# Performance work log

Measured on AMD Instinct MI355X. Metric: run time of the kernel, lower is better.

## Reference

```python
import jax, jax.numpy as jnp
import numpy as np

B, T, D, FF, H, K = 8, 1024, 512, 2048, 8, 15
HD = D // H  # key_dim = d_model // num_heads


def _ln(x, g, b):
    # keras LayerNormalization default epsilon = 1e-3
    m = jnp.mean(x, axis=-1, keepdims=True)
    v = jnp.var(x, axis=-1, keepdims=True)
    return (x - m) * jax.lax.rsqrt(v + 1e-3) * g + b


def setup_inputs() -> dict:
    key = jax.random.key(0)
    ks = iter(jax.random.split(key, 64))

    def rn(shape, s=0.02):
        return jax.random.normal(next(ks), shape, jnp.float32) * s

    p = {}
    p['x'] = jax.random.normal(next(ks), (B, T, D), jnp.float32)
    # ff_pre: LN -> Dense(FF, relu) -> Dense(D)
    p['g1'] = jnp.ones((D,), jnp.float32); p['b1'] = jnp.zeros((D,), jnp.float32)
    p['Wff1'] = rn((D, FF)); p['bff1'] = jnp.zeros((FF,), jnp.float32)
    p['Wff2'] = rn((FF, D)); p['bff2'] = jnp.zeros((D,), jnp.float32)
    # attention norm + MHA projections (keras EinsumDense shapes)
    p['ga'] = jnp.ones((D,), jnp.float32); p['ba'] = jnp.zeros((D,), jnp.float32)
    p['Wq'] = rn((D, H, HD)); p['bq'] = jnp.zeros((H, HD), jnp.float32)
    p['Wk'] = rn((D, H, HD)); p['bk'] = jnp.zeros((H, HD), jnp.float32)
    p['Wv'] = rn((D, H, HD)); p['bv'] = jnp.zeros((H, HD), jnp.float32)
    p['Wo'] = rn((H, HD, D)); p['bo'] = jnp.zeros((D,), jnp.float32)
    # conv branch: LN -> pointwise conv (2D, gelu) -> depthwise conv(k=15) -> BN -> swish -> pointwise conv (D)
    p['gc'] = jnp.ones((D,), jnp.float32); p['bc'] = jnp.zeros((D,), jnp.float32)
    p['Wcp'] = rn((D, 2 * D)); p['bcp'] = jnp.zeros((2 * D,), jnp.float32)
    p['dwk'] = rn((K, 1, 2 * D)); p['dwb'] = jnp.zeros((2 * D,), jnp.float32)
    p['bn_g'] = jnp.ones((2 * D,), jnp.float32); p['bn_b'] = jnp.zeros((2 * D,), jnp.float32)
    p['bn_m'] = jnp.zeros((2 * D,), jnp.float32)
    p['bn_v'] = jnp.ones((2 * D,), jnp.float32)
    p['Wco'] = rn((2 * D, D)); p['bco'] = jnp.zeros((D,), jnp.float32)
    # ff_post
    p['g2'] = jnp.ones((D,), jnp.float32); p['b2'] = jnp.zeros((D,), jnp.float32)
    p['Wf1'] = rn((D, FF)); p['bf1'] = jnp.zeros((FF,), jnp.float32)
    p['Wf2'] = rn((FF, D)); p['bf2'] = jnp.zeros((D,), jnp.float32)
    return p


def reference(x, g1, b1, Wff1, bff1, Wff2, bff2, ga, ba, Wq, bq, Wk, bk, Wv, bv, Wo, bo, gc, bc, Wcp, bcp, dwk, dwb, bn_g, bn_b, bn_m, bn_v, Wco, bco, g2, b2, Wf1, bf1, Wf2, bf2):
    # Macaron FFN (pre), half-step residual applied later
    x_ff = jnp.maximum(_ln(x, g1, b1) @ Wff1 + bff1, 0.0) @ Wff2 + bff2

    # causal multi-head self-attention (cache=None path)
    a = _ln(x, ga, ba)
    q = jnp.einsum('btd,dhk->bthk', a, Wq) + bq
    k = jnp.einsum('btd,dhk->bthk', a, Wk) + bk
    v = jnp.einsum('btd,dhk->bthk', a, Wv) + bv
    scores = jnp.einsum('bqhd,bkhd->bhqk', q, k) / jnp.sqrt(jnp.float32(HD))
    causal = jnp.tril(jnp.ones((T, T), bool))  # [T,T]
    scores = jnp.where(causal, scores, jnp.float32(-1e9))
    w = jax.nn.softmax(scores, axis=-1)
    ctx = jnp.einsum('bhqk,bkhd->bqhd', w, v)
    attn = jnp.einsum('bqhd,hdo->bqo', ctx, Wo) + bo

    x = x + 0.5 * x_ff + attn

    # convolution module: pointwise(gelu) -> causal left-pad -> depthwise -> BN(inference) -> swish -> pointwise
    c = jax.nn.gelu(_ln(x, gc, bc) @ Wcp + bcp, approximate=False)
    c = jnp.pad(c, ((0, 0), (K - 1, 0), (0, 0)))  # causal pad
    c = jax.lax.conv_general_dilated(
        c, dwk, window_strides=(1,), padding='VALID',
        dimension_numbers=('NWC', 'WIO', 'NWC'), feature_group_count=2 * D) + dwb
    c = (c - bn_m) * jax.lax.rsqrt(bn_v + 1e-3) * bn_g + bn_b
    c = c * jax.nn.sigmoid(c)  # swish
    c = c @ Wco + bco
    x = x + c

    # post FFN (full residual)
    x = x + (jnp.maximum(_ln(x, g2, b2) @ Wf1 + bf1, 0.0) @ Wf2 + bf2)
    return x
```

## Files before the change

kernel.cpp:

```cpp
#include <hip/hip_runtime.h>
#include <hip/hip_bf16.h>
#include <math.h>

#define BB 8
#define TT 1024
#define DD 512
#define FFD 2048
#define HH 8
#define HDD 64
#define KW 15
#define MR (BB*TT)
#define QKVN 1536

typedef __attribute__((ext_vector_type(8))) short short8;
typedef __attribute__((ext_vector_type(4))) short short4v;
typedef __attribute__((ext_vector_type(4))) float f32x4;
typedef __hip_bfloat16 bf16;

__device__ __forceinline__ float bf2f(unsigned u16) {
    return __uint_as_float(u16 << 16);
}

__device__ __forceinline__ void async_copy16(const void* g, void* l) {
    __builtin_amdgcn_global_load_lds(
        (const __attribute__((address_space(1))) void*)g,
        (__attribute__((address_space(3))) void*)l, 16, 0, 0);
}

__device__ __forceinline__ float gelu_exact(float v) {
    return 0.5f * v * (1.0f + erff(v * 0.70710678118654752f));
}

__global__ __launch_bounds__(256) void ln_kernel(const float* __restrict__ x,
                                                 const float* __restrict__ g,
                                                 const float* __restrict__ b,
                                                 bf16* __restrict__ out) {
    int wave = (blockIdx.x * blockDim.x + threadIdx.x) >> 6;
    int lane = threadIdx.x & 63;
    if (wave >= MR) return;
    const float* row = x + (size_t)wave * DD;
    float4 v0 = ((const float4*)row)[lane];
    float4 v1 = ((const float4*)row)[64 + lane];
    float s  = v0.x + v0.y + v0.z + v0.w + v1.x + v1.y + v1.z + v1.w;
    float ss = v0.x*v0.x + v0.y*v0.y + v0.z*v0.z + v0.w*v0.w
             + v1.x*v1.x + v1.y*v1.y + v1.z*v1.z + v1.w*v1.w;
    #pragma unroll
    for (int off = 32; off >= 1; off >>= 1) {
        s  += __shfl_xor(s,  off, 64);
        ss += __shfl_xor(ss, off, 64);
    }
    float mean = s * (1.0f / DD);
    float var  = ss * (1.0f / DD) - mean * mean;
    float r    = rsqrtf(var + 1e-3f);
    float4 g0 = ((const float4*)g)[lane];
    float4 g1 = ((const float4*)g)[64 + lane];
    float4 b0 = ((const float4*)b)[lane];
    float4 b1 = ((const float4*)b)[64 + lane];
    alignas(8) bf16 o0[4], o1[4];
    o0[0] = __float2bfloat16((v0.x - mean) * r * g0.x + b0.x);
    o0[1] = __float2bfloat16((v0.y - mean) * r * g0.y + b0.y);
    o0[2] = __float2bfloat16((v0.z - mean) * r * g0.z + b0.z);
    o0[3] = __float2bfloat16((v0.w - mean) * r * g0.w + b0.w);
    o1[0] = __float2bfloat16((v1.x - mean) * r * g1.x + b1.x);
    o1[1] = __float2bfloat16((v1.y - mean) * r * g1.y + b1.y);
    o1[2] = __float2bfloat16((v1.z - mean) * r * g1.z + b1.z);
    o1[3] = __float2bfloat16((v1.w - mean) * r * g1.w + b1.w);
    bf16* orow = out + (size_t)wave * DD;
    *(short4v*)(orow + lane * 4)       = *(const short4v*)o0;
    *(short4v*)(orow + 256 + lane * 4) = *(const short4v*)o1;
}

struct WtPack {
    const float* src[10];
    bf16*        dst[10];
    int          K[10];
    int          lgNT[10];
    float        scale[10];
    int          off[10];
};

__global__ __launch_bounds__(256) void wtrans_all_kernel(WtPack P) {
    __shared__ alignas(16) bf16 T[64][72];
    const int bid = blockIdx.x;
    int e = 0;
    #pragma unroll
    for (int i = 1; i < 10; ++i) e = (bid >= P.off[i]) ? i : e;
    const float* W  = P.src[e];
    bf16*        Wt = P.dst[e];
    const int    K  = P.K[e];
    const int    lg = P.lgNT[e];
    const float  scale = P.scale[e];
    const int local = bid - P.off[e];
    const int bx = local & ((1 << lg) - 1);
    const int by = local >> lg;
    const int k0 = by * 64;
    const int n0 = bx * 64;
    const int N  = (1 << lg) * 64;
    const int tid = threadIdx.x;
    #pragma unroll
    for (int it = 0; it < 4; ++it) {
        int lin = it * 256 + tid;
        int kl  = lin >> 4;
        int nq  = (lin & 15) * 4;
        float4 v = *(const float4*)(W + (size_t)(k0 + kl) * N + n0 + nq);
        T[nq + 0][kl] = __float2bfloat16(v.x * scale);
        T[nq + 1][kl] = __float2bfloat16(v.y * scale);
        T[nq + 2][kl] = __float2bfloat16(v.z * scale);
        T[nq + 3][kl] = __float2bfloat16(v.w * scale);
    }
    __syncthreads();
    #pragma unroll
    for (int it = 0; it < 4; ++it) {
        int lin = it * 256 + tid;
        int nl  = lin >> 4;
        int kq  = (lin & 15) * 4;
        *(short4v*)(Wt + (size_t)(n0 + nl) * K + k0 + kq) = *(const short4v*)&T[nl][kq];
    }
}

__global__ __launch_bounds__(256) void bconcat_kernel(const float* __restrict__ bq,
                                                      const float* __restrict__ bk,
                                                      const float* __restrict__ bv,
                                                      float* __restrict__ dst) {
    int i = blockIdx.x * 256 + threadIdx.x;
    float v = i < 512 ? bq[i] * 0.125f : (i < 1024 ? bk[i - 512] : bv[i - 1024]);
    dst[i] = v;
}

template<int BN, int OP, int RESMODE, int OUTMODE>
__global__ __launch_bounds__(256) void bgemm_kernel(
    const bf16* __restrict__ A,
    const bf16* __restrict__ Bt,
    const float* __restrict__ bias,
    const float* __restrict__ res1,
    const bf16* __restrict__ res2,
    float s2, float oscale,
    void* __restrict__ Cout,
    int N, int Kd, int nxb)
{
    constexpr int NT = BN / 32;
    __shared__ alignas(16) bf16 As[128][64];
    __shared__ alignas(16) bf16 Bs[BN][64];
    const int tid  = threadIdx.x;
    const int w    = tid >> 6;
    const int lane = tid & 63;
    const int quad = lane >> 4;
    const int l16  = lane & 15;
    const int wm   = w >> 1, wn = w & 1;

    const int flat = blockIdx.x;
    const int c8   = flat & 7;
    const int j    = flat >> 3;
    const int jy   = j / nxb;
    const int m0   = (c8 * 8 + jy) * 128;
    const int n0   = (j - jy * nxb) * BN;

    const int srow = lane >> 3;
    const int scol = ((lane & 7) ^ srow) * 8;

    const bf16* Ap = A  + (size_t)(m0 + w * 32 + srow) * Kd + scol;
    const bf16* Bp = Bt + (size_t)(n0 + w * (BN / 4) + srow) * Kd + scol;

    f32x4 acc[4][NT] = {};

    for (int k0 = 0; k0 < Kd; k0 += 64) {
        #pragma unroll
        for (int i = 0; i < 4; ++i)
            async_copy16(Ap + (size_t)(i * 8) * Kd + k0, &As[w * 32 + i * 8][0]);
        #pragma unroll
        for (int i = 0; i < BN / 32; ++i)
            async_copy16(Bp + (size_t)(i * 8) * Kd + k0, &Bs[w * (BN / 4) + i * 8][0]);
        __syncthreads();
        #pragma unroll
        for (int ks = 0; ks < 2; ++ks) {
            short8 af[4], bfr[NT];
            #pragma unroll
            for (int mt = 0; mt < 4; ++mt) {
                const int row = wm * 64 + mt * 16 + l16;
                const int c   = ((ks * 4 + quad) ^ (row & 7)) * 16;
                af[mt] = *(const short8*)((const char*)&As[row][0] + c);
            }
            #pragma unroll
            for (int nt = 0; nt < NT; ++nt) {
                const int col = wn * (BN / 2) + nt * 16 + l16;
                const int c   = ((ks * 4 + quad) ^ (col & 7)) * 16;
                bfr[nt] = *(const short8*)((const char*)&Bs[col][0] + c);
            }
            #pragma unroll
            for (int mt = 0; mt < 4; ++mt)
                #pragma unroll
                for (int nt = 0; nt < NT; ++nt)
                    acc[mt][nt] = __builtin_amdgcn_mfma_f32_16x16x32_bf16(
                        af[mt], bfr[nt], acc[mt][nt], 0, 0, 0);
        }
        __syncthreads();
    }

    const int crow0 = m0 + wm * 64 + quad * 4;
    const int ccol0 = n0 + wn * (BN / 2) + l16;
    #pragma unroll
    for (int nt = 0; nt < NT; ++nt) {
        const int col = ccol0 + nt * 16;
        const float bv = bias[col];
        #pragma unroll
        for (int mt = 0; mt < 4; ++mt) {
            #pragma unroll
            for (int r = 0; r < 4; ++r) {
                const int row = crow0 + mt * 16 + r;
                const size_t off = (size_t)row * N + col;
                float o = acc[mt][nt][r] + bv;
                if (OP == 1)      o = fmaxf(o, 0.f);
                else if (OP == 2) o = gelu_exact(o);
                if (RESMODE >= 1) o += res1[off];
                if (RESMODE == 2) o += s2 * __bfloat162float(res2[off]);
                if (OUTMODE == 0) ((float*)Cout)[off] = o;
                else              ((bf16*)Cout)[off]  = __float2bfloat16(o * oscale);
            }
        }
    }
}

__global__ __launch_bounds__(256) void vtrans_kernel(const bf16* __restrict__ qkv,
                                                     bf16* __restrict__ Vt) {
    __shared__ alignas(16) bf16 tile[64][264];
    int bh = blockIdx.x >> 2;
    int t0 = (blockIdx.x & 3) * 256;
    int b = bh >> 3, h = bh & 7;
    int tid = threadIdx.x;
    #pragma unroll
    for (int it = 0; it < 16; ++it) {
        int lin = it * 256 + tid;
        int tl  = lin >> 4;
        int seg = lin & 15;
        short4v val = *(const short4v*)(qkv + ((size_t)(b * TT) + t0 + tl) * QKVN
                                        + 1024 + h * 64 + seg * 4);
        tile[seg * 4 + 0][tl] = ((const bf16*)&val)[0];
        tile[seg * 4 + 1][tl] = ((const bf16*)&val)[1];
        tile[seg * 4 + 2][tl] = ((const bf16*)&val)[2];
        tile[seg * 4 + 3][tl] = ((const bf16*)&val)[3];
    }
    __syncthreads();
    #pragma unroll
    for (int it = 0; it < 16; ++it) {
        int lin = it * 256 + tid;
        int d   = lin >> 6;
        int tq  = (lin & 63) * 4;
        *(short4v*)(Vt + ((size_t)bh * 64 + d) * TT + t0 + tq) =
            *(const short4v*)&tile[d][tq];
    }
}

__global__ __launch_bounds__(256) void fattn_kernel(
    const bf16* __restrict__ QKV,
    const bf16* __restrict__ Vt,
    bf16* __restrict__ ctx)
{
    __shared__ alignas(16) bf16 Ks[2][64][64];
    __shared__ alignas(16) bf16 Vs[2][64][64];
    const int tid  = threadIdx.x;
    const int w    = tid >> 6;
    const int lane = tid & 63;
    const int quad = lane >> 4;
    const int l16  = lane & 15;
    const int bh   = blockIdx.x & 63;
    const int bi   = 15 - (blockIdx.x >> 6);
    const int b = bh >> 3, h = bh & 7;

    const bf16* Qg = QKV + (size_t)(b * TT) * QKVN + h * 64;
    const bf16* Kg = QKV + (size_t)(b * TT) * QKVN + 512 + h * 64;
    const bf16* Vg = Vt  + (size_t)bh * 64 * TT;

    const int qw = bi * 64 + w * 16;
    short8 qf0 = *(const short8*)(Qg + (size_t)(qw + l16) * QKVN + quad * 8);
    short8 qf1 = *(const short8*)(Qg + (size_t)(qw + l16) * QKVN + 32 + quad * 8);

    const int sgrow  = lane >> 3;
    const int sgchnk = lane & 7;

    f32x4 cacc[4] = {};
    float l_lane = 0.f;
    const int prow_base = ((l16 >> 2) << 3) + (l16 & 3);

    #pragma unroll
    for (int i = 0; i < 2; ++i) {
        const int rowbase = w * 8 + i * 32;
        const int row = rowbase + sgrow;
        const int fR = (row & 3) | (((row >> 3) & 1) << 2);
        const int sc = sgchnk ^ fR;
        async_copy16(Kg + (size_t)row * QKVN + sc * 8, &Ks[0][rowbase][0]);
        async_copy16(Vg + (size_t)row * TT + sc * 8,   &Vs[0][rowbase][0]);
    }

    int buf = 0;
    for (int s = 0; s <= bi; ++s) {
        __syncthreads();
        if (s < bi) {
            const int kn = (s + 1) * 64;
            #pragma unroll
            for (int i = 0; i < 2; ++i) {
                const int rowbase = w * 8 + i * 32;
                const int row = rowbase + sgrow;
                const int fR = (row & 3) | (((row >> 3) & 1) << 2);
                const int sc = sgchnk ^ fR;
                async_copy16(Kg + (size_t)(kn + row) * QKVN + sc * 8, &Ks[buf ^ 1][rowbase][0]);
                async_copy16(Vg + (size_t)row * TT + kn + sc * 8,     &Vs[buf ^ 1][rowbase][0]);
            }
        }
        const int k0 = s * 64;

        f32x4 sT[4];
        #pragma unroll
        for (int s4 = 0; s4 < 4; ++s4) {
            const int prow = prow_base + (s4 >> 1) * 32 + (s4 & 1) * 4;
            const int fR = (prow & 3) | (((prow >> 3) & 1) << 2);
            short8 ka = *(const short8*)&Ks[buf][prow][(quad ^ fR) * 8];
            short8 kb = *(const short8*)&Ks[buf][prow][((4 + quad) ^ fR) * 8];
            f32x4 z = {0.f, 0.f, 0.f, 0.f};
            z = __builtin_amdgcn_mfma_f32_16x16x32_bf16(ka, qf0, z, 0, 0, 0);
            sT[s4] = __builtin_amdgcn_mfma_f32_16x16x32_bf16(kb, qf1, z, 0, 0, 0);
        }

        alignas(16) bf16 pb[16];
        if (s == bi) {
            const int qglob = qw + l16;
            #pragma unroll
            for (int s4 = 0; s4 < 4; ++s4)
                #pragma unroll
                for (int r = 0; r < 4; ++r) {
                    const int key = k0 + (s4 >> 1) * 32 + quad * 8 + (s4 & 1) * 4 + r;
                    const float p = (key <= qglob) ? __expf(sT[s4][r]) : 0.f;
                    l_lane += p;
                    pb[s4 * 4 + r] = __float2bfloat16(p);
                }
        } else {
            #pragma unroll
            for (int s4 = 0; s4 < 4; ++s4)
                #pragma unroll
                for (int r = 0; r < 4; ++r) {
                    const float p = __expf(sT[s4][r]);
                    l_lane += p;
                    pb[s4 * 4 + r] = __float2bfloat16(p);
                }
        }
        const short8 pf0 = *(const short8*)&pb[0];
        const short8 pf1 = *(const short8*)&pb[8];

        #pragma unroll
        for (int g = 0; g < 4; ++g) {
            const int vrow = g * 16 + l16;
            const int fR = (vrow & 3) | (((vrow >> 3) & 1) << 2);
            short8 va = *(const short8*)&Vs[buf][vrow][(quad ^ fR) * 8];
            short8 vb = *(const short8*)&Vs[buf][vrow][((4 + quad) ^ fR) * 8];
            cacc[g] = __builtin_amdgcn_mfma_f32_16x16x32_bf16(va, pf0, cacc[g], 0, 0, 0);
            cacc[g] = __builtin_amdgcn_mfma_f32_16x16x32_bf16(vb, pf1, cacc[g], 0, 0, 0);
        }
        buf ^= 1;
    }

    l_lane += __shfl_xor(l_lane, 16, 64);
    l_lane += __shfl_xor(l_lane, 32, 64);
    const float inv = 1.0f / l_lane;

    bf16* Cb = ctx + (size_t)(b * TT + qw + l16) * DD + h * 64;
    #pragma unroll
    for (int g = 0; g < 4; ++g) {
        alignas(8) bf16 o[4];
        #pragma unroll
        for (int r = 0; r < 4; ++r) o[r] = __float2bfloat16(cacc[g][r] * inv);
        *(short4v*)(Cb + g * 16 + quad * 4) = *(const short4v*)o;
    }
}

__global__ __launch_bounds__(256) void dwconv_kernel(const bf16* __restrict__ c1,
                                                     const float* __restrict__ dwk,
                                                     const float* __restrict__ dwb,
                                                     const float* __restrict__ bn_g,
                                                     const float* __restrict__ bn_b,
                                                     const float* __restrict__ bn_m,
                                                     const float* __restrict__ bn_v,
                                                     bf16* __restrict__ out) {
    const int C2 = 2 * DD;
    const int lin = blockIdx.x * 256 + threadIdx.x;
    const int chp = lin & 511;
    const int ch  = chp << 1;
    const int tch = lin >> 9;
    const int row0 = tch << 3;
    const int t0   = row0 & (TT - 1);

    float w0[KW], w1[KW];
    #pragma unroll
    for (int i = 0; i < KW; ++i) {
        w0[i] = dwk[i * C2 + ch];
        w1[i] = dwk[i * C2 + ch + 1];
    }
    const float a0 = rsqrtf(bn_v[ch] + 1e-3f) * bn_g[ch];
    const float a1 = rsqrtf(bn_v[ch + 1] + 1e-3f) * bn_g[ch + 1];
    const float c0 = (dwb[ch] - bn_m[ch]) * a0 + bn_b[ch];
    const float c1v = (dwb[ch + 1] - bn_m[ch + 1]) * a1 + bn_b[ch + 1];

    float x0[22], x1[22];
    if (t0 >= KW - 1) {
        #pragma unroll
        for (int i = 0; i < 22; ++i) {
            unsigned u = *(const unsigned*)(c1 + (size_t)(row0 - (KW - 1) + i) * C2 + ch);
            x0[i] = bf2f(u & 0xffff);
            x1[i] = bf2f(u >> 16);
        }
    } else {
        #pragma unroll
        for (int i = 0; i < 22; ++i) {
            unsigned u = 0;
            if (t0 - (KW - 1) + i >= 0)
                u = *(const unsigned*)(c1 + (size_t)(row0 - (KW - 1) + i) * C2 + ch);
            x0[i] = bf2f(u & 0xffff);
            x1[i] = bf2f(u >> 16);
        }
    }

    #pragma unroll
    for (int j = 0; j < 8; ++j) {
        float s0 = 0.f, s1 = 0.f;
        #pragma unroll
        for (int i = 0; i < KW; ++i) {
            s0 += x0[j + i] * w0[i];
            s1 += x1[j + i] * w1[i];
        }
        s0 = s0 * a0 + c0;
        s1 = s1 * a1 + c1v;
        s0 = s0 / (1.f + __expf(-s0));
        s1 = s1 / (1.f + __expf(-s1));
        alignas(4) bf16 ob[2] = {__float2bfloat16(s0), __float2bfloat16(s1)};
        *(unsigned*)(out + (size_t)(row0 + j) * C2 + ch) = *(const unsigned*)ob;
    }
}

extern "C" void kernel_launch(void* const* d_in, const int* in_sizes, int n_in,
                              void* d_out, int out_size, void* d_ws, size_t ws_size,
                              hipStream_t stream) {
    const float* x    = (const float*)d_in[0];
    const float* g1   = (const float*)d_in[1];
    const float* b1   = (const float*)d_in[2];
    const float* Wff1 = (const float*)d_in[3];
    const float* bff1 = (const float*)d_in[4];
    const float* Wff2 = (const float*)d_in[5];
    const float* bff2 = (const float*)d_in[6];
    const float* ga   = (const float*)d_in[7];
    const float* ba   = (const float*)d_in[8];
    const float* Wq   = (const float*)d_in[9];
    const float* bq   = (const float*)d_in[10];
    const float* Wk   = (const float*)d_in[11];
    const float* bk   = (const float*)d_in[12];
    const float* Wv   = (const float*)d_in[13];
    const float* bv   = (const float*)d_in[14];
    const float* Wo   = (const float*)d_in[15];
    const float* bo   = (const float*)d_in[16];
    const float* gc   = (const float*)d_in[17];
    const float* bc   = (const float*)d_in[18];
    const float* Wcp  = (const float*)d_in[19];
    const float* bcp  = (const float*)d_in[20];
    const float* dwk  = (const float*)d_in[21];
    const float* dwb  = (const float*)d_in[22];
    const float* bn_g = (const float*)d_in[23];
    const float* bn_b = (const float*)d_in[24];
    const float* bn_m = (const float*)d_in[25];
    const float* bn_v = (const float*)d_in[26];
    const float* Wco  = (const float*)d_in[27];
    const float* bco  = (const float*)d_in[28];
    const float* g2   = (const float*)d_in[29];
    const float* b2   = (const float*)d_in[30];
    const float* Wf1  = (const float*)d_in[31];
    const float* bf1  = (const float*)d_in[32];
    const float* Wf2  = (const float*)d_in[33];
    const float* bf2  = (const float*)d_in[34];

    float* out = (float*)d_out;

    char* p = (char*)d_ws;
    bf16* lnb   = (bf16*)p;  p += (size_t)MR * DD * 2;
    bf16* qkvb  = (bf16*)p;  p += (size_t)MR * QKVN * 2;
    bf16* Vtb   = (bf16*)p;  p += (size_t)MR * DD * 2;
    bf16* ctxb  = (bf16*)p;  p += (size_t)MR * DD * 2;
    bf16* xffb  = (bf16*)p;  p += (size_t)MR * DD * 2;
    bf16* bigb  = (bf16*)p;  p += (size_t)MR * FFD * 2;
    bf16* c2b   = (bf16*)p;  p += (size_t)MR * 1024 * 2;
    bf16* Wff1t = (bf16*)p;  p += (size_t)FFD * DD * 2;
    bf16* Wff2t = (bf16*)p;  p += (size_t)DD * FFD * 2;
    bf16* Wqkvt = (bf16*)p;  p += (size_t)QKVN * DD * 2;
    bf16* Wot   = (bf16*)p;  p += (size_t)DD * DD * 2;
    bf16* Wcpt  = (bf16*)p;  p += (size_t)1024 * DD * 2;
    bf16* Wcot  = (bf16*)p;  p += (size_t)DD * 1024 * 2;
    bf16* Wf1t  = (bf16*)p;  p += (size_t)FFD * DD * 2;
    bf16* Wf2t  = (bf16*)p;  p += (size_t)DD * FFD * 2;
    float* bqkv = (float*)p; p += QKVN * 4;

    dim3 blk(256);
    dim3 ln_grid(MR / 4);

    WtPack P;
    auto set = [&](int i, const float* s, bf16* d, int K, int N, float sc, int off) {
        P.src[i] = s; P.dst[i] = d; P.K[i] = K; P.scale[i] = sc; P.off[i] = off;
        int nt = N / 64, lg = 0; while ((1 << lg) < nt) ++lg; P.lgNT[i] = lg;
    };
    set(0, Wff1, Wff1t, DD,  FFD, 1.f,    0);
    set(1, Wff2, Wff2t, FFD, DD,  1.f,    256);
    set(2, Wq,   Wqkvt,                DD, DD, 0.125f, 512);
    set(3, Wk,   Wqkvt + (size_t)512 * DD,  DD, DD, 1.f, 576);
    set(4, Wv,   Wqkvt + (size_t)1024 * DD, DD, DD, 1.f, 640);
    set(5, Wo,   Wot,   DD,  DD,  1.f,    704);
    set(6, Wcp,  Wcpt,  DD,  1024, 1.f,   768);
    set(7, Wco,  Wcot,  1024, DD, 1.f,    896);
    set(8, Wf1,  Wf1t,  DD,  FFD, 1.f,    1024);
    set(9, Wf2,  Wf2t,  FFD, DD,  1.f,    1280);
    wtrans_all_kernel<<<dim3(1536), blk, 0, stream>>>(P);
    bconcat_kernel<<<dim3(QKVN / 256), blk, 0, stream>>>(bq, bk, bv, bqkv);

    ln_kernel<<<ln_grid, blk, 0, stream>>>(x, g1, b1, lnb);
    bgemm_kernel<128, 1, 0, 1><<<dim3(16 * 64), blk, 0, stream>>>(
        lnb, Wff1t, bff1, nullptr, nullptr, 0.f, 1.f, bigb, FFD, DD, 16);
    bgemm_kernel<64, 0, 0, 1><<<dim3(8 * 64), blk, 0, stream>>>(
        bigb, Wff2t, bff2, nullptr, nullptr, 0.f, 1.f, xffb, DD, FFD, 8);
    ln_kernel<<<ln_grid, blk, 0, stream>>>(x, ga, ba, lnb);
    bgemm_kernel<128, 0, 0, 1><<<dim3(12 * 64), blk, 0, stream>>>(
        lnb, Wqkvt, bqkv, nullptr, nullptr, 0.f, 1.f, qkvb, QKVN, DD, 12);
    vtrans_kernel<<<dim3(64 * 4), blk, 0, stream>>>(qkvb, Vtb);
    fattn_kernel<<<dim3(64 * 16), blk, 0, stream>>>(qkvb, Vtb, ctxb);
    bgemm_kernel<64, 0, 2, 0><<<dim3(8 * 64), blk, 0, stream>>>(
        ctxb, Wot, bo, x, xffb, 0.5f, 1.f, out, DD, DD, 8);
    ln_kernel<<<ln_grid, blk, 0, stream>>>(out, gc, bc, lnb);
    bgemm_kernel<128, 2, 0, 1><<<dim3(8 * 64), blk, 0, stream>>>(
        lnb, Wcpt, bcp, nullptr, nullptr, 0.f, 1.f, bigb, 1024, DD, 8);
    dwconv_kernel<<<dim3(MR * 512 / 8 / 256), blk, 0, stream>>>(
        bigb, dwk, dwb, bn_g, bn_b, bn_m, bn_v, c2b);
    bgemm_kernel<64, 0, 1, 0><<<dim3(8 * 64), blk, 0, stream>>>(
        c2b, Wcot, bco, out, nullptr, 0.f, 1.f, out, DD, 1024, 8);
    ln_kernel<<<ln_grid, blk, 0, stream>>>(out, g2, b2, lnb);
    bgemm_kernel<128, 1, 0, 1><<<dim3(16 * 64), blk, 0, stream>>>(
        lnb, Wf1t, bf1, nullptr, nullptr, 0.f, 1.f, bigb, FFD, DD, 16);
    bgemm_kernel<64, 0, 1, 0><<<dim3(8 * 64), blk, 0, stream>>>(
        bigb, Wf2t, bf2, out, nullptr, 0.f, 1.f, out, DD, FFD, 8);
}
```

Measured before the change: 399.1 us.

## Fuse LN pair, bias concat, V transpose; process two query tiles per attention block

```diff
diff --git a/kernel.cpp b/kernel.cpp
--- a/kernel.cpp
+++ b/kernel.cpp
@@ -29,6 +29,72 @@
 
 __device__ __forceinline__ float gelu_exact(float v) {
     return 0.5f * v * (1.0f + erff(v * 0.70710678118654752f));
+}
+
+__global__ __launch_bounds__(256) void ln_dual_kernel(const float* __restrict__ x,
+                                                      const float* __restrict__ g1,
+                                                      const float* __restrict__ b1,
+                                                      const float* __restrict__ ga,
+                                                      const float* __restrict__ ba,
+                                                      bf16* __restrict__ o1,
+                                                      bf16* __restrict__ o2) {
+    int wave = (blockIdx.x * blockDim.x + threadIdx.x) >> 6;
+    int lane = threadIdx.x & 63;
+    if (wave >= MR) return;
+    const float* row = x + (size_t)wave * DD;
+    float4 v0 = ((const float4*)row)[lane];
+    float4 v1 = ((const float4*)row)[64 + lane];
+    float s  = v0.x + v0.y + v0.z + v0.w + v1.x + v1.y + v1.z + v1.w;
+    float ss = v0.x*v0.x + v0.y*v0.y + v0.z*v0.z + v0.w*v0.w
+             + v1.x*v1.x + v1.y*v1.y + v1.z*v1.z + v1.w*v1.w;
+    #pragma unroll
+    for (int off = 32; off >= 1; off >>= 1) {
+        s  += __shfl_xor(s,  off, 64);
+        ss += __shfl_xor(ss, off, 64);
+    }
+    float mean = s * (1.0f / DD);
+    float var  = ss * (1.0f / DD) - mean * mean;
+    float r    = rsqrtf(var + 1e-3f);
+    float n0x = (v0.x - mean) * r, n0y = (v0.y - mean) * r,
+          n0z = (v0.z - mean) * r, n0w = (v0.w - mean) * r;
+    float n1x = (v1.x - mean) * r, n1y = (v1.y - mean) * r,
+          n1z = (v1.z - mean) * r, n1w = (v1.w - mean) * r;
+    {
+        float4 g0 = ((const float4*)g1)[lane];
+        float4 gg1 = ((const float4*)g1)[64 + lane];
+        float4 b0 = ((const float4*)b1)[lane];
+        float4 bb1 = ((const float4*)b1)[64 + lane];
+        alignas(8) bf16 oo0[4], oo1[4];
+        oo0[0] = __float2bfloat16(n0x * g0.x + b0.x);
+        oo0[1] = __float2bfloat16(n0y * g0.y + b0.y);
+        oo0[2] = __float2bfloat16(n0z * g0.z + b0.z);
+        oo0[3] = __float2bfloat16(n0w * g0.w + b0.w);
+        oo1[0] = __float2bfloat16(n1x * gg1.x + bb1.x);
+        oo1[1] = __float2bfloat16(n1y * gg1.y + bb1.y);
+        oo1[2] = __float2bfloat16(n1z * gg1.z + bb1.z);
+        oo1[3] = __float2bfloat16(n1w * gg1.w + bb1.w);
+        bf16* orow = o1 + (size_t)wave * DD;
+        *(short4v*)(orow + lane * 4)       = *(const short4v*)oo0;
+        *(short4v*)(orow + 256 + lane * 4) = *(const short4v*)oo1;
+    }
+    {
+        float4 g0 = ((const float4*)ga)[lane];
+        float4 gg1 = ((const float4*)ga)[64 + lane];
+        float4 b0 = ((const float4*)ba)[lane];
+        float4 bb1 = ((const float4*)ba)[64 + lane];
+        alignas(8) bf16 oo0[4], oo1[4];
+        oo0[0] = __float2bfloat16(n0x * g0.x + b0.x);
+        oo0[1] = __float2bfloat16(n0y * g0.y + b0.y);
+        oo0[2] = __float2bfloat16(n0z * g0.z + b0.z);
+        oo0[3] = __float2bfloat16(n0w * g0.w + b0.w);
+        oo1[0] = __float2bfloat16(n1x * gg1.x + bb1.x);
+        oo1[1] = __float2bfloat16(n1y * gg1.y + bb1.y);
+        oo1[2] = __float2bfloat16(n1z * gg1.z + bb1.z);
+        oo1[3] = __float2bfloat16(n1w * gg1.w + bb1.w);
+        bf16* orow = o2 + (size_t)wave * DD;
+        *(short4v*)(orow + lane * 4)       = *(const short4v*)oo0;
+        *(short4v*)(orow + 256 + lane * 4) = *(const short4v*)oo1;
+    }
 }
 
 __global__ __launch_bounds__(256) void ln_kernel(const float* __restrict__ x,
@@ -77,11 +143,23 @@
     int          lgNT[10];
     float        scale[10];
     int          off[10];
+    const float* bq; const float* bk; const float* bv;
+    float*       bdst;
 };
 
 __global__ __launch_bounds__(256) void wtrans_all_kernel(WtPack P) {
     __shared__ alignas(16) bf16 T[64][72];
     const int bid = blockIdx.x;
+    if (bid >= 1536) {
+        #pragma unroll
+        for (int it = 0; it < 6; ++it) {
+            int i = it * 256 + threadIdx.x;
+            float v = i < 512 ? P.bq[i] * 0.125f
+                              : (i < 1024 ? P.bk[i - 512] : P.bv[i - 1024]);
+            P.bdst[i] = v;
+        }
+        return;
+    }
     int e = 0;
     #pragma unroll
     for (int i = 1; i < 10; ++i) e = (bid >= P.off[i]) ? i : e;
@@ -118,15 +196,6 @@
     }
 }
 
-__global__ __launch_bounds__(256) void bconcat_kernel(const float* __restrict__ bq,
-                                                      const float* __restrict__ bk,
-                                                      const float* __restrict__ bv,
-                                                      float* __restrict__ dst) {
-    int i = blockIdx.x * 256 + threadIdx.x;
-    float v = i < 512 ? bq[i] * 0.125f : (i < 1024 ? bk[i - 512] : bv[i - 1024]);
-    dst[i] = v;
-}
-
 template<int BN, int OP, int RESMODE, int OUTMODE>
 __global__ __launch_bounds__(256) void bgemm_kernel(
     const bf16* __restrict__ A,
@@ -134,6 +203,7 @@
     const float* __restrict__ bias,
     const float* __restrict__ res1,
     const bf16* __restrict__ res2,
+    bf16* __restrict__ aux,
     float s2, float oscale,
     void* __restrict__ Cout,
     int N, int Kd, int nxb)
@@ -204,49 +274,38 @@
         const float bv = bias[col];
         #pragma unroll
         for (int mt = 0; mt < 4; ++mt) {
-            #pragma unroll
-            for (int r = 0; r < 4; ++r) {
-                const int row = crow0 + mt * 16 + r;
-                const size_t off = (size_t)row * N + col;
-                float o = acc[mt][nt][r] + bv;
-                if (OP == 1)      o = fmaxf(o, 0.f);
-                else if (OP == 2) o = gelu_exact(o);
-                if (RESMODE >= 1) o += res1[off];
-                if (RESMODE == 2) o += s2 * __bfloat162float(res2[off]);
-                if (OUTMODE == 0) ((float*)Cout)[off] = o;
-                else              ((bf16*)Cout)[off]  = __float2bfloat16(o * oscale);
+            if (OUTMODE == 2) {
+                alignas(8) bf16 o4[4];
+                #pragma unroll
+                for (int r = 0; r < 4; ++r)
+                    o4[r] = __float2bfloat16((acc[mt][nt][r] + bv) * oscale);
+                if (col < 1024) {
+                    #pragma unroll
+                    for (int r = 0; r < 4; ++r)
+                        ((bf16*)Cout)[(size_t)(crow0 + mt * 16 + r) * N + col] = o4[r];
+                } else {
+                    const int dg   = col - 1024;
+                    const int rowt = crow0 + mt * 16;
+                    const int b2   = rowt >> 10, t0 = rowt & 1023;
+                    const int bh2  = b2 * 8 + (dg >> 6), d = dg & 63;
+                    *(short4v*)(aux + ((size_t)bh2 * 64 + d) * TT + t0) =
+                        *(const short4v*)o4;
+                }
+            } else {
+                #pragma unroll
+                for (int r = 0; r < 4; ++r) {
+                    const int row = crow0 + mt * 16 + r;
+                    const size_t off = (size_t)row * N + col;
+                    float o = acc[mt][nt][r] + bv;
+                    if (OP == 1)      o = fmaxf(o, 0.f);
+                    else if (OP == 2) o = gelu_exact(o);
+                    if (RESMODE >= 1) o += res1[off];
+                    if (RESMODE == 2) o += s2 * __bfloat162float(res2[off]);
+                    if (OUTMODE == 0) ((float*)Cout)[off] = o;
+                    else              ((bf16*)Cout)[off]  = __float2bfloat16(o * oscale);
+                }
             }
         }
-    }
-}
-
-__global__ __launch_bounds__(256) void vtrans_kernel(const bf16* __restrict__ qkv,
-                                                     bf16* __restrict__ Vt) {
-    __shared__ alignas(16) bf16 tile[64][264];
-    int bh = blockIdx.x >> 2;
-    int t0 = (blockIdx.x & 3) * 256;
-    int b = bh >> 3, h = bh & 7;
-    int tid = threadIdx.x;
-    #pragma unroll
-    for (int it = 0; it < 16; ++it) {
-        int lin = it * 256 + tid;
-        int tl  = lin >> 4;
-        int seg = lin & 15;
-        short4v val = *(const short4v*)(qkv + ((size_t)(b * TT) + t0 + tl) * QKVN
-                                        + 1024 + h * 64 + seg * 4);
-        tile[seg * 4 + 0][tl] = ((const bf16*)&val)[0];
-        tile[seg * 4 + 1][tl] = ((const bf16*)&val)[1];
-        tile[seg * 4 + 2][tl] = ((const bf16*)&val)[2];
-        tile[seg * 4 + 3][tl] = ((const bf16*)&val)[3];
-    }
-    __syncthreads();
-    #pragma unroll
-    for (int it = 0; it < 16; ++it) {
-        int lin = it * 256 + tid;
-        int d   = lin >> 6;
-        int tq  = (lin & 63) * 4;
-        *(short4v*)(Vt + ((size_t)bh * 64 + d) * TT + t0 + tq) =
-            *(const short4v*)&tile[d][tq];
     }
 }
 
@@ -263,23 +322,27 @@
     const int quad = lane >> 4;
     const int l16  = lane & 15;
     const int bh   = blockIdx.x & 63;
-    const int bi   = 15 - (blockIdx.x >> 6);
+    const int bi   = 7 - (blockIdx.x >> 6);
     const int b = bh >> 3, h = bh & 7;
 
     const bf16* Qg = QKV + (size_t)(b * TT) * QKVN + h * 64;
     const bf16* Kg = QKV + (size_t)(b * TT) * QKVN + 512 + h * 64;
     const bf16* Vg = Vt  + (size_t)bh * 64 * TT;
 
-    const int qw = bi * 64 + w * 16;
-    short8 qf0 = *(const short8*)(Qg + (size_t)(qw + l16) * QKVN + quad * 8);
-    short8 qf1 = *(const short8*)(Qg + (size_t)(qw + l16) * QKVN + 32 + quad * 8);
+    const int qL = bi * 128 + w * 16;
+    const int qH = qL + 64;
+    short8 qfL0 = *(const short8*)(Qg + (size_t)(qL + l16) * QKVN + quad * 8);
+    short8 qfL1 = *(const short8*)(Qg + (size_t)(qL + l16) * QKVN + 32 + quad * 8);
+    short8 qfH0 = *(const short8*)(Qg + (size_t)(qH + l16) * QKVN + quad * 8);
+    short8 qfH1 = *(const short8*)(Qg + (size_t)(qH + l16) * QKVN + 32 + quad * 8);
 
     const int sgrow  = lane >> 3;
     const int sgchnk = lane & 7;
 
-    f32x4 cacc[4] = {};
-    float l_lane = 0.f;
+    f32x4 caccL[4] = {}, caccH[4] = {};
+    float lL = 0.f, lH = 0.f;
     const int prow_base = ((l16 >> 2) << 3) + (l16 & 3);
+    const int smax = 2 * bi + 1;
 
     #pragma unroll
     for (int i = 0; i < 2; ++i) {
@@ -292,9 +355,9 @@
     }
 
     int buf = 0;
-    for (int s = 0; s <= bi; ++s) {
+    for (int s = 0; s <= smax; ++s) {
         __syncthreads();
-        if (s < bi) {
+        if (s < smax) {
             const int kn = (s + 1) * 64;
             #pragma unroll
             for (int i = 0; i < 2; ++i) {
@@ -307,43 +370,74 @@
             }
         }
         const int k0 = s * 64;
-
-        f32x4 sT[4];
+        const bool doL = (s < smax);
+
+        f32x4 sTL[4], sTH[4];
         #pragma unroll
         for (int s4 = 0; s4 < 4; ++s4) {
             const int prow = prow_base + (s4 >> 1) * 32 + (s4 & 1) * 4;
             const int fR = (prow & 3) | (((prow >> 3) & 1) << 2);
             short8 ka = *(const short8*)&Ks[buf][prow][(quad ^ fR) * 8];
             short8 kb = *(const short8*)&Ks[buf][prow][((4 + quad) ^ fR) * 8];
-            f32x4 z = {0.f, 0.f, 0.f, 0.f};
-            z = __builtin_amdgcn_mfma_f32_16x16x32_bf16(ka, qf0, z, 0, 0, 0);
-            sT[s4] = __builtin_amdgcn_mfma_f32_16x16x32_bf16(kb, qf1, z, 0, 0, 0);
-        }
-
-        alignas(16) bf16 pb[16];
-        if (s == bi) {
-            const int qglob = qw + l16;
+            f32x4 zH = {0.f, 0.f, 0.f, 0.f};
+            zH = __builtin_amdgcn_mfma_f32_16x16x32_bf16(ka, qfH0, zH, 0, 0, 0);
+            sTH[s4] = __builtin_amdgcn_mfma_f32_16x16x32_bf16(kb, qfH1, zH, 0, 0, 0);
+            if (doL) {
+                f32x4 zL = {0.f, 0.f, 0.f, 0.f};
+                zL = __builtin_amdgcn_mfma_f32_16x16x32_bf16(ka, qfL0, zL, 0, 0, 0);
+                sTL[s4] = __builtin_amdgcn_mfma_f32_16x16x32_bf16(kb, qfL1, zL, 0, 0, 0);
+            }
+        }
+
+        alignas(16) bf16 pbH[16], pbL[16];
+        if (s == smax) {
+            const int qg = qH + l16;
             #pragma unroll
             for (int s4 = 0; s4 < 4; ++s4)
                 #pragma unroll
                 for (int r = 0; r < 4; ++r) {
                     const int key = k0 + (s4 >> 1) * 32 + quad * 8 + (s4 & 1) * 4 + r;
-                    const float p = (key <= qglob) ? __expf(sT[s4][r]) : 0.f;
-                    l_lane += p;
-                    pb[s4 * 4 + r] = __float2bfloat16(p);
+                    const float p = (key <= qg) ? __expf(sTH[s4][r]) : 0.f;
+                    lH += p;
+                    pbH[s4 * 4 + r] = __float2bfloat16(p);
                 }
         } else {
             #pragma unroll
             for (int s4 = 0; s4 < 4; ++s4)
                 #pragma unroll
                 for (int r = 0; r < 4; ++r) {
-                    const float p = __expf(sT[s4][r]);
-                    l_lane += p;
-                    pb[s4 * 4 + r] = __float2bfloat16(p);
+                    const float p = __expf(sTH[s4][r]);
+                    lH += p;
+                    pbH[s4 * 4 + r] = __float2bfloat16(p);
                 }
         }
-        const short8 pf0 = *(const short8*)&pb[0];
-        const short8 pf1 = *(const short8*)&pb[8];
+        if (doL) {
+            if (s == smax - 1) {
+                const int qg = qL + l16;
+                #pragma unroll
+                for (int s4 = 0; s4 < 4; ++s4)
+                    #pragma unroll
+                    for (int r = 0; r < 4; ++r) {
+                        const int key = k0 + (s4 >> 1) * 32 + quad * 8 + (s4 & 1) * 4 + r;
+                        const float p = (key <= qg) ? __expf(sTL[s4][r]) : 0.f;
+                        lL += p;
+                        pbL[s4 * 4 + r] = __float2bfloat16(p);
+                    }
+            } else {
+                #pragma unroll
+                for (int s4 = 0; s4 < 4; ++s4)
+                    #pragma unroll
+                    for (int r = 0; r < 4; ++r) {
+                        const float p = __expf(sTL[s4][r]);
+                        lL += p;
+                        pbL[s4 * 4 + r] = __float2bfloat16(p);
+                    }
+            }
+        }
+        const short8 pfH0 = *(const short8*)&pbH[0];
+        const short8 pfH1 = *(const short8*)&pbH[8];
+        const short8 pfL0 = *(const short8*)&pbL[0];
+        const short8 pfL1 = *(const short8*)&pbL[8];
 
         #pragma unroll
         for (int g = 0; g < 4; ++g) {
@@ -351,23 +445,35 @@
             const int fR = (vrow & 3) | (((vrow >> 3) & 1) << 2);
             short8 va = *(const short8*)&Vs[buf][vrow][(quad ^ fR) * 8];
             short8 vb = *(const short8*)&Vs[buf][vrow][((4 + quad) ^ fR) * 8];
-            cacc[g] = __builtin_amdgcn_mfma_f32_16x16x32_bf16(va, pf0, cacc[g], 0, 0, 0);
-            cacc[g] = __builtin_amdgcn_mfma_f32_16x16x32_bf16(vb, pf1, cacc[g], 0, 0, 0);
+            caccH[g] = __builtin_amdgcn_mfma_f32_16x16x32_bf16(va, pfH0, caccH[g], 0, 0, 0);
+            caccH[g] = __builtin_amdgcn_mfma_f32_16x16x32_bf16(vb, pfH1, caccH[g], 0, 0, 0);
+            if (doL) {
+                caccL[g] = __builtin_amdgcn_mfma_f32_16x16x32_bf16(va, pfL0, caccL[g], 0, 0, 0);
+                caccL[g] = __builtin_amdgcn_mfma_f32_16x16x32_bf16(vb, pfL1, caccL[g], 0, 0, 0);
+            }
         }
         buf ^= 1;
     }
 
-    l_lane += __shfl_xor(l_lane, 16, 64);
-    l_lane += __shfl_xor(l_lane, 32, 64);
-    const float inv = 1.0f / l_lane;
-
-    bf16* Cb = ctx + (size_t)(b * TT + qw + l16) * DD + h * 64;
+    lL += __shfl_xor(lL, 16, 64);
+    lL += __shfl_xor(lL, 32, 64);
+    lH += __shfl_xor(lH, 16, 64);
+    lH += __shfl_xor(lH, 32, 64);
+    const float invL = 1.0f / lL;
+    const float invH = 1.0f / lH;
+
+    bf16* CbL = ctx + (size_t)(b * TT + qL + l16) * DD + h * 64;
+    bf16* CbH = ctx + (size_t)(b * TT + qH + l16) * DD + h * 64;
     #pragma unroll
     for (int g = 0; g < 4; ++g) {
-        alignas(8) bf16 o[4];
-        #pragma unroll
-        for (int r = 0; r < 4; ++r) o[r] = __float2bfloat16(cacc[g][r] * inv);
-        *(short4v*)(Cb + g * 16 + quad * 4) = *(const short4v*)o;
+        alignas(8) bf16 oL[4], oH[4];
+        #pragma unroll
+        for (int r = 0; r < 4; ++r) {
+            oL[r] = __float2bfloat16(caccL[g][r] * invL);
+            oH[r] = __float2bfloat16(caccH[g][r] * invH);
+        }
+        *(short4v*)(CbL + g * 16 + quad * 4) = *(const short4v*)oL;
+        *(short4v*)(CbH + g * 16 + quad * 4) = *(const short4v*)oH;
     }
 }
 
@@ -477,6 +583,7 @@
 
     char* p = (char*)d_ws;
     bf16* lnb   = (bf16*)p;  p += (size_t)MR * DD * 2;
+    bf16* lnab  = (bf16*)p;  p += (size_t)MR * DD * 2;
     bf16* qkvb  = (bf16*)p;  p += (size_t)MR * QKVN * 2;
     bf16* Vtb   = (bf16*)p;  p += (size_t)MR * DD * 2;
     bf16* ctxb  = (bf16*)p;  p += (size_t)MR * DD * 2;
@@ -511,31 +618,29 @@
     set(7, Wco,  Wcot,  1024, DD, 1.f,    896);
     set(8, Wf1,  Wf1t,  DD,  FFD, 1.f,    1024);
     set(9, Wf2,  Wf2t,  FFD, DD,  1.f,    1280);
-    wtrans_all_kernel<<<dim3(1536), blk, 0, stream>>>(P);
-    bconcat_kernel<<<dim3(QKVN / 256), blk, 0, stream>>>(bq, bk, bv, bqkv);
-
-    ln_kernel<<<ln_grid, blk, 0, stream>>>(x, g1, b1, lnb);
+    P.bq = bq; P.bk = bk; P.bv = bv; P.bdst = bqkv;
+    wtrans_all_kernel<<<dim3(1537), blk, 0, stream>>>(P);
+
+    ln_dual_kernel<<<ln_grid, blk, 0, stream>>>(x, g1, b1, ga, ba, lnb, lnab);
     bgemm_kernel<128, 1, 0, 1><<<dim3(16 * 64), blk, 0, stream>>>(
-        lnb, Wff1t, bff1, nullptr, nullptr, 0.f, 1.f, bigb, FFD, DD, 16);
+        lnb, Wff1t, bff1, nullptr, nullptr, nullptr, 0.f, 1.f, bigb, FFD, DD, 16);
     bgemm_kernel<64, 0, 0, 1><<<dim3(8 * 64), blk, 0, stream>>>(
-        bigb, Wff2t, bff2, nullptr, nullptr, 0.f, 1.f, xffb, DD, FFD, 8);
-    ln_kernel<<<ln_grid, blk, 0, stream>>>(x, ga, ba, lnb);
-    bgemm_kernel<128, 0, 0, 1><<<dim3(12 * 64), blk, 0, stream>>>(
-        lnb, Wqkvt, bqkv, nullptr, nullptr, 0.f, 1.f, qkvb, QKVN, DD, 12);
-    vtrans_kernel<<<dim3(64 * 4), blk, 0, stream>>>(qkvb, Vtb);
-    fattn_kernel<<<dim3(64 * 16), blk, 0, stream>>>(qkvb, Vtb, ctxb);
+        bigb, Wff2t, bff2, nullptr, nullptr, nullptr, 0.f, 1.f, xffb, DD, FFD, 8);
+    bgemm_kernel<128, 0, 0, 2><<<dim3(12 * 64), blk, 0, stream>>>(
+        lnab, Wqkvt, bqkv, nullptr, nullptr, Vtb, 0.f, 1.f, qkvb, QKVN, DD, 12);
+    fattn_kernel<<<dim3(64 * 8), blk, 0, stream>>>(qkvb, Vtb, ctxb);
     bgemm_kernel<64, 0, 2, 0><<<dim3(8 * 64), blk, 0, stream>>>(
-        ctxb, Wot, bo, x, xffb, 0.5f, 1.f, out, DD, DD, 8);
+        ctxb, Wot, bo, x, xffb, nullptr, 0.5f, 1.f, out, DD, DD, 8);
     ln_kernel<<<ln_grid, blk, 0, stream>>>(out, gc, bc, lnb);
     bgemm_kernel<128, 2, 0, 1><<<dim3(8 * 64), blk, 0, stream>>>(
-        lnb, Wcpt, bcp, nullptr, nullptr, 0.f, 1.f, bigb, 1024, DD, 8);
+        lnb, Wcpt, bcp, nullptr, nullptr, nullptr, 0.f, 1.f, bigb, 1024, DD, 8);
     dwconv_kernel<<<dim3(MR * 512 / 8 / 256), blk, 0, stream>>>(
         bigb, dwk, dwb, bn_g, bn_b, bn_m, bn_v, c2b);
     bgemm_kernel<64, 0, 1, 0><<<dim3(8 * 64), blk, 0, stream>>>(
-        c2b, Wcot, bco, out, nullptr, 0.f, 1.f, out, DD, 1024, 8);
+        c2b, Wcot, bco, out, nullptr, nullptr, 0.f, 1.f, out, DD, 1024, 8);
     ln_kernel<<<ln_grid, blk, 0, stream>>>(out, g2, b2, lnb);
     bgemm_kernel<128, 1, 0, 1><<<dim3(16 * 64), blk, 0, stream>>>(
-        lnb, Wf1t, bf1, nullptr, nullptr, 0.f, 1.f, bigb, FFD, DD, 16);
+        lnb, Wf1t, bf1, nullptr, nullptr, nullptr, 0.f, 1.f, bigb, FFD, DD, 16);
     bgemm_kernel<64, 0, 1, 0><<<dim3(8 * 64), blk, 0, stream>>>(
-        bigb, Wf2t, bf2, out, nullptr, 0.f, 1.f, out, DD, FFD, 8);
-}
+        bigb, Wf2t, bf2, out, nullptr, nullptr, 0.f, 1.f, out, DD, FFD, 8);
+}
```

Measured after the change: 394.7 us. About the same (-1.1%).
